# Kernel tuning notes

Measured on AMD Instinct MI355X. Metric: run time of the kernel, lower is better.

Reference implementation:

```python
import jax, jax.numpy as jnp
import numpy as np

B, S, D, H, E, K = 8, 8192, 256, 1024, 8, 2


def setup_inputs() -> dict:
    key = jax.random.key(0)
    ks = jax.random.split(key, 7)
    s_in = 1.0 / np.sqrt(D)
    s_hid = 1.0 / np.sqrt(H)
    return {
        "x": jax.random.normal(ks[0], (B, S, D), dtype=jnp.float32),
        "Wg": jax.random.uniform(ks[1], (E, D), jnp.float32, -s_in, s_in),
        "bg": jax.random.uniform(ks[2], (E,), jnp.float32, -s_in, s_in),
        "W1": jax.random.uniform(ks[3], (E, H, D), jnp.float32, -s_in, s_in),
        "b1": jax.random.uniform(ks[4], (E, H), jnp.float32, -s_in, s_in),
        "W2": jax.random.uniform(ks[5], (E, D, H), jnp.float32, -s_hid, s_hid),
        "b2": jax.random.uniform(ks[6], (E, D), jnp.float32, -s_hid, s_hid),
    }


def reference(x, Wg, bg, W1, b1, W2, b2):
    # gate: [B,S,E]
    gate_scores = jnp.einsum("bsd,ed->bse", x, Wg) + bg
    topk_scores, topk_idx = jax.lax.top_k(gate_scores, K)  # [B,S,K]
    topk_probs = jax.nn.softmax(topk_scores, axis=-1)      # [B,S,K]
    # combine weight per expert: sum over top-k slots of prob * one_hot(idx)
    combine = jnp.sum(topk_probs[..., None] * jax.nn.one_hot(topk_idx, E, dtype=x.dtype), axis=-2)  # [B,S,E]
    out = jnp.zeros_like(x)
    for e in range(E):  # small fixed loop over experts
        h = jax.nn.relu(jnp.einsum("bsd,hd->bsh", x, W1[e]) + b1[e])
        y = jnp.einsum("bsh,dh->bsd", h, W2[e]) + b2[e]
        out = out + combine[..., e:e + 1] * y
    return out
```

## Files before the change

kernel.cpp:

```cpp
#include <hip/hip_runtime.h>
#include <hip/hip_bf16.h>

#define T_TOKENS 65536
#define D_DIM 256
#define H_DIM 1024
#define E_NUM 8
#define MT 128
#define HC 32
#define NCHUNK 32
#define GTB 64

typedef __attribute__((ext_vector_type(4))) float f32x4;
typedef __attribute__((ext_vector_type(8))) short s16x8;
typedef __attribute__((ext_vector_type(4))) unsigned int u32x4;
typedef __attribute__((ext_vector_type(4))) unsigned short u16x4;
typedef __attribute__((address_space(3))) unsigned int lds_u32;
typedef const __attribute__((address_space(1))) unsigned int glb_u32;

#define MFMA __builtin_amdgcn_mfma_f32_16x16x32_bf16

__device__ __forceinline__ unsigned short f2bf(float f){
  union { float f; unsigned u; } v; v.f = f;
  unsigned r = v.u + 0x7FFFu + ((v.u >> 16) & 1u);
  return (unsigned short)(r >> 16);
}
__device__ __forceinline__ float bf2f(unsigned short h){
  return __uint_as_float((unsigned)h << 16);
}
__device__ __forceinline__ unsigned cvtpk(float lo, float hi){
  unsigned r;
  asm("v_cvt_pk_bf16_f32 %0, %1, %2" : "=v"(r) : "v"(lo), "v"(hi));
  return r;
}
__device__ __forceinline__ unsigned long long pack4(f32x4 v){
  return (unsigned long long)f2bf(v.x)
       | ((unsigned long long)f2bf(v.y) << 16)
       | ((unsigned long long)f2bf(v.z) << 32)
       | ((unsigned long long)f2bf(v.w) << 48);
}

__device__ __forceinline__ void cvt_unit(int i, const float* __restrict__ W1,
                                         const float* __restrict__ W2,
                                         char* __restrict__ wsw){
  const int N1 = (E_NUM * H_DIM * D_DIM) / 4;
  unsigned long long pk;
  size_t off;
  if (i < N1){
    pk = pack4(((const f32x4*)W1)[i]);
    int idx = i << 2;
    int e  = idx >> 18;
    int h  = (idx >> 8) & (H_DIM - 1);
    int d0 = idx & (D_DIM - 1);
    int c = h >> 5, r = h & 31;
    off = ((size_t)(e * NCHUNK + c) << 15)
        + (size_t)(((r << 9) + (d0 << 1)) ^ ((r & 7) << 4));
  } else {
    pk = pack4(((const f32x4*)W2)[i - N1]);
    int idx = (i - N1) << 2;
    int e  = idx >> 18;
    int d  = (idx >> 10) & (D_DIM - 1);
    int h0 = idx & (H_DIM - 1);
    int c  = h0 >> 5;
    int mi = (h0 >> 4) & 1, qjs = (h0 >> 2) & 3;
    int s2 = qjs * 16 + mi * 8;
    off = ((size_t)(e * NCHUNK + c) << 15) + 16384
        + (size_t)((d << 6) + (s2 ^ (((d >> 1) & 3) << 4)));
  }
  *(unsigned long long*)(wsw + off) = pk;
}

__global__ __launch_bounds__(256) void gate_kernel(
    const float* __restrict__ x, const float* __restrict__ Wg,
    const float* __restrict__ bg,
    const float* __restrict__ W1, const float* __restrict__ W2,
    char* __restrict__ wsw,
    int* __restrict__ counts, int* __restrict__ tok_ids, float* __restrict__ rrec)
{
  __shared__ int lcnt[E_NUM];
  __shared__ int lbase[E_NUM];
  __shared__ unsigned char aexp[GTB * 2];
  __shared__ short         apos[GTB * 2];

  int tid = threadIdx.x, wave = tid >> 6, lane = tid & 63;

  int gthr = blockIdx.x * 256 + tid;
#pragma unroll
  for (int j = 0; j < 4; ++j)
    cvt_unit(gthr + j * ((T_TOKENS / GTB) * 256), W1, W2, wsw);

  if (tid < E_NUM) lcnt[tid] = 0;
  __syncthreads();

  int t0 = blockIdx.x * GTB;
#pragma unroll 1
  for (int i = 0; i < GTB / 4; ++i){
    int tl = wave * (GTB / 4) + i;
    int t = t0 + tl;
    f32x4 xv = *(const f32x4*)(x + (size_t)t * D_DIM + 4*lane);
    float s[E_NUM];
#pragma unroll
    for (int e = 0; e < E_NUM; ++e){
      f32x4 w = *(const f32x4*)(Wg + e*D_DIM + 4*lane);
      s[e] = xv.x*w.x + xv.y*w.y + xv.z*w.z + xv.w*w.w;
    }
#pragma unroll
    for (int off = 32; off; off >>= 1){
#pragma unroll
      for (int e = 0; e < E_NUM; ++e) s[e] += __shfl_xor(s[e], off);
    }
#pragma unroll
    for (int e = 0; e < E_NUM; ++e) s[e] += bg[e];
    int e0 = 0; float v0 = s[0];
#pragma unroll
    for (int e = 1; e < E_NUM; ++e) if (s[e] > v0){ v0 = s[e]; e0 = e; }
    int e1 = -1; float v1 = -3.4e38f;
#pragma unroll
    for (int e = 0; e < E_NUM; ++e){
      if (e == e0) continue;
      if (s[e] > v1){ v1 = s[e]; e1 = e; }
    }
    float ex = __expf(v1 - v0);
    float inv = 1.f / (1.f + ex);
    float p0 = inv, p1 = ex * inv;
    if (lane == 0){
      int li = tl * 2;
      int pos0 = atomicAdd(&lcnt[e0], 1);
      int pos1 = atomicAdd(&lcnt[e1], 1);
      aexp[li]   = (unsigned char)e0; apos[li]   = (short)pos0;
      aexp[li+1] = (unsigned char)e1; apos[li+1] = (short)pos1;
      f32x4 rr; rr.x = p0; rr.y = p1; rr.z = (float)e0; rr.w = (float)e1;
      *(f32x4*)(rrec + (size_t)t * 4) = rr;
    }
  }
  __syncthreads();
  if (tid < E_NUM) lbase[tid] = atomicAdd(counts + tid*16, lcnt[tid]);
  __syncthreads();
  if (tid < GTB * 2){
    int t = t0 + (tid >> 1);
    int e = aexp[tid];
    int idx = lbase[e] + apos[tid];
    tok_ids[e*T_TOKENS + idx] = t | ((tid & 1) << 16);
  }
}

__global__ __launch_bounds__(256, 2) void ffn_kernel(
  const float* __restrict__ x, const char* __restrict__ wsw,
  const float* __restrict__ b1,
  const int* __restrict__ counts, const int* __restrict__ tok_ids,
  unsigned short* __restrict__ yslot)
{
  const int e    = blockIdx.x & 7;
  const int tile = blockIdx.x >> 3;
  const int cnt  = counts[e * 16];
  const int base = tile * MT;
  if (base >= cnt) return;

  __shared__ __align__(1024) unsigned short Ws[2][16384];
  __shared__ __align__(16)   float b1s[H_DIM];
  __shared__ int sTok[MT];

  const int tid = threadIdx.x, wave = tid >> 6, lane = tid & 63;
  const int mrow = lane & 15, qj = lane >> 4;
  const char* wexp = wsw + ((size_t)(e * NCHUNK) << 15);

  auto stage = [&](int c, int buf){
    const char* src = wexp + ((size_t)c << 15);
    char* dst = (char*)&Ws[buf][0];
#pragma unroll
    for (int i = 0; i < 8; ++i){
      int ub = i * 4096 + wave * 1024;
      __builtin_amdgcn_global_load_lds(
        (glb_u32*)(src + ub + lane * 16),
        (lds_u32*)(dst + ub), 16, 0, 0);
    }
  };

  if (tid < MT){
    int idx = base + tid;
    sTok[tid] = (idx < cnt) ? tok_ids[e*T_TOKENS + idx] : -1;
  }
  *(f32x4*)&b1s[tid * 4] = ((const f32x4*)(b1 + e*H_DIM))[tid];
  __syncthreads();

  stage(0, 0);

  s16x8 afr[2][8];
#pragma unroll
  for (int ti = 0; ti < 2; ++ti){
    int ent = sTok[wave*32 + ti*16 + mrow];
    int tk = ent & 0xFFFF;
    const f32x4* src = (const f32x4*)(x + (size_t)(ent < 0 ? 0 : tk) * D_DIM);
#pragma unroll
    for (int k = 0; k < 8; ++k){
      f32x4 a = src[k*8 + qj*2];
      f32x4 b = src[k*8 + qj*2 + 1];
      s16x8 f;
      f[0]=(short)f2bf(a.x); f[1]=(short)f2bf(a.y); f[2]=(short)f2bf(a.z); f[3]=(short)f2bf(a.w);
      f[4]=(short)f2bf(b.x); f[5]=(short)f2bf(b.y); f[6]=(short)f2bf(b.z); f[7]=(short)f2bf(b.w);
      if (ent < 0) f = (s16x8)(short)0;
      afr[ti][k] = f;
    }
  }

  const int w1base = mrow*512 + ((qj*16) ^ ((mrow & 3) << 4));
  const int w1sb   = (mrow >> 2) & 1;
  const int w2base = 16384 + mrow*64 + ((qj*16) ^ (((mrow >> 1) & 3) << 4));

  asm volatile("s_waitcnt vmcnt(0) lgkmcnt(0)" ::: "memory");
  __builtin_amdgcn_s_barrier();

  f32x4 yacc[16][2];
#pragma unroll
  for (int m = 0; m < 16; ++m){
    yacc[m][0] = (f32x4){0.f,0.f,0.f,0.f};
    yacc[m][1] = (f32x4){0.f,0.f,0.f,0.f};
  }

  int buf = 0;
#pragma unroll 1
  for (int c = 0; c < NCHUNK; ++c){
    if (c + 1 < NCHUNK) stage(c + 1, buf ^ 1);
    const char* Wb = (const char*)&Ws[buf][0];

    f32x4 hacc[2][2];
    hacc[0][0] = (f32x4){0.f,0.f,0.f,0.f}; hacc[0][1] = (f32x4){0.f,0.f,0.f,0.f};
    hacc[1][0] = (f32x4){0.f,0.f,0.f,0.f}; hacc[1][1] = (f32x4){0.f,0.f,0.f,0.f};
#pragma unroll
    for (int ks = 0; ks < 8; ++ks){
      int ko = ((ks ^ w1sb) << 6);
      s16x8 w1a = *(const s16x8*)(Wb + w1base + ko);
      s16x8 w1b = *(const s16x8*)(Wb + 8192 + w1base + ko);
      hacc[0][0] = MFMA(w1a, afr[0][ks], hacc[0][0], 0, 0, 0);
      hacc[0][1] = MFMA(w1a, afr[1][ks], hacc[0][1], 0, 0, 0);
      hacc[1][0] = MFMA(w1b, afr[0][ks], hacc[1][0], 0, 0, 0);
      hacc[1][1] = MFMA(w1b, afr[1][ks], hacc[1][1], 0, 0, 0);
    }

    f32x4 bv0 = *(const f32x4*)&b1s[c*32 + qj*4];
    f32x4 bv1 = *(const f32x4*)&b1s[c*32 + 16 + qj*4];
    s16x8 pb0, pb1;
    {
      f32x4 h0 = hacc[0][0], h1 = hacc[1][0];
      h0.x = fmaxf(h0.x + bv0.x, 0.f); h0.y = fmaxf(h0.y + bv0.y, 0.f);
      h0.z = fmaxf(h0.z + bv0.z, 0.f); h0.w = fmaxf(h0.w + bv0.w, 0.f);
      h1.x = fmaxf(h1.x + bv1.x, 0.f); h1.y = fmaxf(h1.y + bv1.y, 0.f);
      h1.z = fmaxf(h1.z + bv1.z, 0.f); h1.w = fmaxf(h1.w + bv1.w, 0.f);
      u32x4 pw;
      pw.x = cvtpk(h0.x, h0.y); pw.y = cvtpk(h0.z, h0.w);
      pw.z = cvtpk(h1.x, h1.y); pw.w = cvtpk(h1.z, h1.w);
      pb0 = __builtin_bit_cast(s16x8, pw);
    }
    {
      f32x4 h0 = hacc[0][1], h1 = hacc[1][1];
      h0.x = fmaxf(h0.x + bv0.x, 0.f); h0.y = fmaxf(h0.y + bv0.y, 0.f);
      h0.z = fmaxf(h0.z + bv0.z, 0.f); h0.w = fmaxf(h0.w + bv0.w, 0.f);
      h1.x = fmaxf(h1.x + bv1.x, 0.f); h1.y = fmaxf(h1.y + bv1.y, 0.f);
      h1.z = fmaxf(h1.z + bv1.z, 0.f); h1.w = fmaxf(h1.w + bv1.w, 0.f);
      u32x4 pw;
      pw.x = cvtpk(h0.x, h0.y); pw.y = cvtpk(h0.z, h0.w);
      pw.z = cvtpk(h1.x, h1.y); pw.w = cvtpk(h1.z, h1.w);
      pb1 = __builtin_bit_cast(s16x8, pw);
    }

#pragma unroll
    for (int m = 0; m < 16; ++m){
      s16x8 w2f = *(const s16x8*)(Wb + w2base + m*1024);
      yacc[m][0] = MFMA(w2f, pb0, yacc[m][0], 0, 0, 0);
      yacc[m][1] = MFMA(w2f, pb1, yacc[m][1], 0, 0, 0);
    }

    asm volatile("s_waitcnt vmcnt(0)" ::: "memory");
    __builtin_amdgcn_s_barrier();
    buf ^= 1;
  }

#pragma unroll
  for (int ti = 0; ti < 2; ++ti){
    int ent = sTok[wave*32 + ti*16 + mrow];
    if (ent < 0) continue;
    int slot = ((ent & 0xFFFF) << 1) | ((ent >> 16) & 1);
    unsigned short* dst = yslot + (size_t)slot * 256;
#pragma unroll
    for (int m = 0; m < 16; ++m){
      unsigned lo = cvtpk(yacc[m][ti][0], yacc[m][ti][1]);
      unsigned hi = cvtpk(yacc[m][ti][2], yacc[m][ti][3]);
      *(unsigned*)(dst + m*16 + qj*4)     = lo;
      *(unsigned*)(dst + m*16 + qj*4 + 2) = hi;
    }
  }
}

__global__ __launch_bounds__(256) void combine_kernel(
    const float* __restrict__ rrec, const float* __restrict__ b2,
    float* __restrict__ out)
{
  int t = blockIdx.x * 4 + (threadIdx.x >> 6);
  int lane = threadIdx.x & 63;
  f32x4 rr = *(const f32x4*)(rrec + (size_t)t * 4);
  float p0 = rr.x, p1 = rr.y;
  int e0 = (int)rr.z, e1 = (int)rr.w;
  const u16x4* s0 = (const u16x4*)((const unsigned short*)out + (size_t)t * 512);
  u16x4 a = s0[lane];
  u16x4 b = s0[64 + lane];
  f32x4 z0 = *(const f32x4*)(b2 + e0*D_DIM + 4*lane);
  f32x4 z1 = *(const f32x4*)(b2 + e1*D_DIM + 4*lane);
  f32x4 o;
  o.x = p0*(bf2f(a.x) + z0.x) + p1*(bf2f(b.x) + z1.x);
  o.y = p0*(bf2f(a.y) + z0.y) + p1*(bf2f(b.y) + z1.y);
  o.z = p0*(bf2f(a.z) + z0.z) + p1*(bf2f(b.z) + z1.z);
  o.w = p0*(bf2f(a.w) + z0.w) + p1*(bf2f(b.w) + z1.w);
  *(f32x4*)(out + (size_t)t * D_DIM + 4*lane) = o;
}

extern "C" void kernel_launch(void* const* d_in, const int* in_sizes, int n_in,
                              void* d_out, int out_size, void* d_ws, size_t ws_size,
                              hipStream_t stream) {
  const float* x  = (const float*)d_in[0];
  const float* Wg = (const float*)d_in[1];
  const float* bg = (const float*)d_in[2];
  const float* W1 = (const float*)d_in[3];
  const float* b1 = (const float*)d_in[4];
  const float* W2 = (const float*)d_in[5];
  const float* b2 = (const float*)d_in[6];
  float* out = (float*)d_out;
  char* ws = (char*)d_ws;

  char*  wsw     = ws;
  int*   counts  = (int*)  (ws + 8388608);
  int*   tok_ids = (int*)  (ws + 8389632);
  float* rrec    = (float*)(ws + 10486784);

  hipMemsetAsync(counts, 0, 512, stream);
  gate_kernel<<<T_TOKENS/GTB, 256, 0, stream>>>(x, Wg, bg, W1, W2, wsw,
                                                counts, tok_ids, rrec);
  ffn_kernel<<<E_NUM * (T_TOKENS/MT), 256, 0, stream>>>(x, wsw, b1, counts, tok_ids,
                                                        (unsigned short*)d_out);
  combine_kernel<<<T_TOKENS/4, 256, 0, stream>>>(rrec, b2, out);
}
```

Before: 258.3 us.

## Split W1/W2 LDS staging to fit three blocks per CU and reorder prefetch

Replaces the double-buffered combined weight buffer with a single W1 buffer and a double-buffered W2 buffer. This cuts LDS per block so three blocks can reside per CU, and launch bounds are raised to 3 to match. The next chunk's prefetch moves to after the W1 GEMM, with partial vmcnt waits so W1 loads are awaited before W2. MFMA phases are wrapped in s_setprio to favour the math waves. The higher occupancy target tightens the VGPR budget, which risks spilling given the large accumulator and A-fragment arrays, and the added mid-loop barrier may expose load latency.

```diff
diff --git a/kernel.cpp b/kernel.cpp
--- a/kernel.cpp
+++ b/kernel.cpp
@@ -143,7 +143,7 @@
   }
 }
 
-__global__ __launch_bounds__(256, 2) void ffn_kernel(
+__global__ __launch_bounds__(256, 3) void ffn_kernel(
   const float* __restrict__ x, const char* __restrict__ wsw,
   const float* __restrict__ b1,
   const int* __restrict__ counts, const int* __restrict__ tok_ids,
@@ -155,7 +155,8 @@
   const int base = tile * MT;
   if (base >= cnt) return;
 
-  __shared__ __align__(1024) unsigned short Ws[2][16384];
+  __shared__ __align__(1024) unsigned short W1s[8192];
+  __shared__ __align__(1024) unsigned short W2s[2][8192];
   __shared__ __align__(16)   float b1s[H_DIM];
   __shared__ int sTok[MT];
 
@@ -163,11 +164,21 @@
   const int mrow = lane & 15, qj = lane >> 4;
   const char* wexp = wsw + ((size_t)(e * NCHUNK) << 15);
 
-  auto stage = [&](int c, int buf){
+  auto stage_w1 = [&](int c){
     const char* src = wexp + ((size_t)c << 15);
-    char* dst = (char*)&Ws[buf][0];
-#pragma unroll
-    for (int i = 0; i < 8; ++i){
+#pragma unroll
+    for (int i = 0; i < 4; ++i){
+      int ub = i * 4096 + wave * 1024;
+      __builtin_amdgcn_global_load_lds(
+        (glb_u32*)(src + ub + lane * 16),
+        (lds_u32*)((char*)W1s + ub), 16, 0, 0);
+    }
+  };
+  auto stage_w2 = [&](int c, int buf){
+    const char* src = wexp + ((size_t)c << 15) + 16384;
+    char* dst = (char*)&W2s[buf][0];
+#pragma unroll
+    for (int i = 0; i < 4; ++i){
       int ub = i * 4096 + wave * 1024;
       __builtin_amdgcn_global_load_lds(
         (glb_u32*)(src + ub + lane * 16),
@@ -182,7 +193,8 @@
   *(f32x4*)&b1s[tid * 4] = ((const f32x4*)(b1 + e*H_DIM))[tid];
   __syncthreads();
 
-  stage(0, 0);
+  stage_w1(0);
+  stage_w2(0, 0);
 
   s16x8 afr[2][8];
 #pragma unroll
@@ -204,9 +216,9 @@
 
   const int w1base = mrow*512 + ((qj*16) ^ ((mrow & 3) << 4));
   const int w1sb   = (mrow >> 2) & 1;
-  const int w2base = 16384 + mrow*64 + ((qj*16) ^ (((mrow >> 1) & 3) << 4));
-
-  asm volatile("s_waitcnt vmcnt(0) lgkmcnt(0)" ::: "memory");
+  const int w2base = mrow*64 + ((qj*16) ^ (((mrow >> 1) & 3) << 4));
+
+  asm volatile("s_waitcnt vmcnt(4)" ::: "memory");
   __builtin_amdgcn_s_barrier();
 
   f32x4 yacc[16][2];
@@ -216,12 +228,12 @@
     yacc[m][1] = (f32x4){0.f,0.f,0.f,0.f};
   }
 
-  int buf = 0;
+  int cur = 0;
 #pragma unroll 1
   for (int c = 0; c < NCHUNK; ++c){
-    if (c + 1 < NCHUNK) stage(c + 1, buf ^ 1);
-    const char* Wb = (const char*)&Ws[buf][0];
-
+    const char* Wb = (const char*)W1s;
+
+    __builtin_amdgcn_s_setprio(1);
     f32x4 hacc[2][2];
     hacc[0][0] = (f32x4){0.f,0.f,0.f,0.f}; hacc[0][1] = (f32x4){0.f,0.f,0.f,0.f};
     hacc[1][0] = (f32x4){0.f,0.f,0.f,0.f}; hacc[1][1] = (f32x4){0.f,0.f,0.f,0.f};
@@ -261,17 +273,29 @@
       pw.z = cvtpk(h1.x, h1.y); pw.w = cvtpk(h1.z, h1.w);
       pb1 = __builtin_bit_cast(s16x8, pw);
     }
-
+    __builtin_amdgcn_s_setprio(0);
+
+    asm volatile("s_waitcnt vmcnt(0)" ::: "memory");
+    __builtin_amdgcn_s_barrier();
+
+    if (c + 1 < NCHUNK){
+      stage_w1(c + 1);
+      stage_w2(c + 1, cur ^ 1);
+    }
+
+    __builtin_amdgcn_s_setprio(1);
+    const char* W2c = (const char*)&W2s[cur][0];
 #pragma unroll
     for (int m = 0; m < 16; ++m){
-      s16x8 w2f = *(const s16x8*)(Wb + w2base + m*1024);
+      s16x8 w2f = *(const s16x8*)(W2c + w2base + m*1024);
       yacc[m][0] = MFMA(w2f, pb0, yacc[m][0], 0, 0, 0);
       yacc[m][1] = MFMA(w2f, pb1, yacc[m][1], 0, 0, 0);
     }
-
-    asm volatile("s_waitcnt vmcnt(0)" ::: "memory");
+    __builtin_amdgcn_s_setprio(0);
+
+    asm volatile("s_waitcnt vmcnt(4)" ::: "memory");
     __builtin_amdgcn_s_barrier();
-    buf ^= 1;
+    cur ^= 1;
   }
 
 #pragma unroll
```

Result: slower. 550.0 us (+112.9%).

## Load W2 fragments directly from global into registers, halve LDS weight staging

Applied to the files above, without the earlier changes.

The W2 half of each weight chunk is re-laid out in the pre-swizzled buffer so every lane reads its MFMA fragment with a contiguous 16-byte global load. Those fragments are register-prefetched (four ahead) instead of being staged through LDS. LDS staging now covers only W1, which halves LDS use per block and could allow more blocks per CU. s_setprio hints are placed around the MFMA sections. The cost is more direct global/L2 traffic per wave and exposed load latency inside the W2 loop.

```diff
diff --git a/kernel.cpp b/kernel.cpp
--- a/kernel.cpp
+++ b/kernel.cpp
@@ -57,14 +57,14 @@
   } else {
     pk = pack4(((const f32x4*)W2)[i - N1]);
     int idx = (i - N1) << 2;
-    int e  = idx >> 18;
-    int d  = (idx >> 10) & (D_DIM - 1);
-    int h0 = idx & (H_DIM - 1);
-    int c  = h0 >> 5;
-    int mi = (h0 >> 4) & 1, qjs = (h0 >> 2) & 3;
-    int s2 = qjs * 16 + mi * 8;
+    int e   = idx >> 18;
+    int d   = (idx >> 10) & (D_DIM - 1);
+    int h0  = idx & (H_DIM - 1);
+    int c   = h0 >> 5;
+    int h32 = h0 & 31;
+    int mi = (h32 >> 4) & 1, qj = (h32 >> 2) & 3;
     off = ((size_t)(e * NCHUNK + c) << 15) + 16384
-        + (size_t)((d << 6) + (s2 ^ (((d >> 1) & 3) << 4)));
+        + (size_t)(((d >> 4) << 10) + ((qj * 16 + (d & 15)) << 4) + (mi << 3));
   }
   *(unsigned long long*)(wsw + off) = pk;
 }
@@ -155,7 +155,7 @@
   const int base = tile * MT;
   if (base >= cnt) return;
 
-  __shared__ __align__(1024) unsigned short Ws[2][16384];
+  __shared__ __align__(1024) unsigned short W1s[2][8192];
   __shared__ __align__(16)   float b1s[H_DIM];
   __shared__ int sTok[MT];
 
@@ -163,11 +163,11 @@
   const int mrow = lane & 15, qj = lane >> 4;
   const char* wexp = wsw + ((size_t)(e * NCHUNK) << 15);
 
-  auto stage = [&](int c, int buf){
+  auto stage_w1 = [&](int c, int buf){
     const char* src = wexp + ((size_t)c << 15);
-    char* dst = (char*)&Ws[buf][0];
-#pragma unroll
-    for (int i = 0; i < 8; ++i){
+    char* dst = (char*)&W1s[buf][0];
+#pragma unroll
+    for (int i = 0; i < 4; ++i){
       int ub = i * 4096 + wave * 1024;
       __builtin_amdgcn_global_load_lds(
         (glb_u32*)(src + ub + lane * 16),
@@ -182,7 +182,7 @@
   *(f32x4*)&b1s[tid * 4] = ((const f32x4*)(b1 + e*H_DIM))[tid];
   __syncthreads();
 
-  stage(0, 0);
+  stage_w1(0, 0);
 
   s16x8 afr[2][8];
 #pragma unroll
@@ -204,7 +204,6 @@
 
   const int w1base = mrow*512 + ((qj*16) ^ ((mrow & 3) << 4));
   const int w1sb   = (mrow >> 2) & 1;
-  const int w2base = 16384 + mrow*64 + ((qj*16) ^ (((mrow >> 1) & 3) << 4));
 
   asm volatile("s_waitcnt vmcnt(0) lgkmcnt(0)" ::: "memory");
   __builtin_amdgcn_s_barrier();
@@ -219,9 +218,14 @@
   int buf = 0;
 #pragma unroll 1
   for (int c = 0; c < NCHUNK; ++c){
-    if (c + 1 < NCHUNK) stage(c + 1, buf ^ 1);
-    const char* Wb = (const char*)&Ws[buf][0];
-
+    if (c + 1 < NCHUNK) stage_w1(c + 1, buf ^ 1);
+
+    const s16x8* w2c = (const s16x8*)(wexp + (((size_t)c) << 15) + 16384) + lane;
+    s16x8 wfa = w2c[0], wfb = w2c[64], wfc = w2c[128], wfd = w2c[192];
+
+    const char* Wb = (const char*)&W1s[buf][0];
+
+    __builtin_amdgcn_s_setprio(1);
     f32x4 hacc[2][2];
     hacc[0][0] = (f32x4){0.f,0.f,0.f,0.f}; hacc[0][1] = (f32x4){0.f,0.f,0.f,0.f};
     hacc[1][0] = (f32x4){0.f,0.f,0.f,0.f}; hacc[1][1] = (f32x4){0.f,0.f,0.f,0.f};
@@ -235,6 +239,7 @@
       hacc[1][0] = MFMA(w1b, afr[0][ks], hacc[1][0], 0, 0, 0);
       hacc[1][1] = MFMA(w1b, afr[1][ks], hacc[1][1], 0, 0, 0);
     }
+    __builtin_amdgcn_s_setprio(0);
 
     f32x4 bv0 = *(const f32x4*)&b1s[c*32 + qj*4];
     f32x4 bv1 = *(const f32x4*)&b1s[c*32 + 16 + qj*4];
@@ -262,12 +267,24 @@
       pb1 = __builtin_bit_cast(s16x8, pw);
     }
 
-#pragma unroll
-    for (int m = 0; m < 16; ++m){
-      s16x8 w2f = *(const s16x8*)(Wb + w2base + m*1024);
-      yacc[m][0] = MFMA(w2f, pb0, yacc[m][0], 0, 0, 0);
-      yacc[m][1] = MFMA(w2f, pb1, yacc[m][1], 0, 0, 0);
-    }
+    __builtin_amdgcn_s_setprio(1);
+#pragma unroll
+    for (int m = 0; m < 16; m += 4){
+      s16x8 f0 = wfa, f1 = wfb, f2 = wfc, f3 = wfd;
+      if (m + 4 < 16){
+        wfa = w2c[(m + 4) * 64]; wfb = w2c[(m + 5) * 64];
+        wfc = w2c[(m + 6) * 64]; wfd = w2c[(m + 7) * 64];
+      }
+      yacc[m+0][0] = MFMA(f0, pb0, yacc[m+0][0], 0, 0, 0);
+      yacc[m+0][1] = MFMA(f0, pb1, yacc[m+0][1], 0, 0, 0);
+      yacc[m+1][0] = MFMA(f1, pb0, yacc[m+1][0], 0, 0, 0);
+      yacc[m+1][1] = MFMA(f1, pb1, yacc[m+1][1], 0, 0, 0);
+      yacc[m+2][0] = MFMA(f2, pb0, yacc[m+2][0], 0, 0, 0);
+      yacc[m+2][1] = MFMA(f2, pb1, yacc[m+2][1], 0, 0, 0);
+      yacc[m+3][0] = MFMA(f3, pb0, yacc[m+3][0], 0, 0, 0);
+      yacc[m+3][1] = MFMA(f3, pb1, yacc[m+3][1], 0, 0, 0);
+    }
+    __builtin_amdgcn_s_setprio(0);
 
     asm volatile("s_waitcnt vmcnt(0)" ::: "memory");
     __builtin_amdgcn_s_barrier();
```

New measurement: 408.7 us. 1.58x slower.
